# Performance work log

Hardware: AMD Instinct MI355X
Metric: run time of the kernel (lower is better)

The kernel has to match this reference:

```python
import jax, jax.numpy as jnp
import numpy as np

DIM = 512

def setup_inputs() -> dict:
    key = jax.random.key(0)
    k1, k2, k3 = jax.random.split(key, 3)
    context = jax.random.normal(k1, (64, 1024, DIM), dtype=jnp.float32)
    query = jax.random.normal(k2, (64, 128, DIM), dtype=jnp.float32)
    # nn.Linear(3*dim, 1, bias=False) weight, flattened to a (3*dim,) vector
    w0 = jax.random.normal(k3, (3 * DIM,), dtype=jnp.float32) * (1.0 / np.sqrt(3 * DIM))
    return {"context": context, "query": query, "w0": w0}

def reference(context, query, w0):
    # Trilinear similarity: sim[b,i,j] = w_c.c_i + w_q.q_j + w_m.(c_i*q_j)
    # (equivalent to Linear(concat([c, q, c*q])) without materializing the concat)
    d = context.shape[-1]
    wc, wq, wm = w0[:d], w0[d:2 * d], w0[2 * d:]
    sim = (context @ wc)[:, :, None] \
        + (query @ wq)[:, None, :] \
        + jnp.einsum('bid,bjd->bij', context * wm, query)  # (B, ctx, q)
    # Original: softmax over trailing dim of size 1 -> all ones (faithful to the bug)
    S = jnp.ones_like(sim)                 # (B, ctx, q)
    SS = jax.nn.softmax(sim, axis=1)       # softmax over context dim
    A = S @ query                          # (B, ctx, d)
    B = S @ jnp.swapaxes(SS, 1, 2) @ context  # (B, ctx, d)
    return (A, B)
```

## Files before the change

### kernel.cpp

```cpp
#include <hip/hip_runtime.h>
#include <hip/hip_bf16.h>

#define NB   64
#define NC   1024
#define NQ   128
#define DIMD 512
#define BK   64
#define NKC  (DIMD / BK)
#define LDK  (BK + 8)
#define TM   128
#define NTILE (NC / TM)

using short8  = __attribute__((ext_vector_type(8))) short;
using short4v = __attribute__((ext_vector_type(4))) short;
using f32x4   = __attribute__((ext_vector_type(4))) float;
typedef __fp16 half2v __attribute__((ext_vector_type(2)));

__device__ inline float dot4(float4 a, float4 b) {
    return a.x * b.x + a.y * b.y + a.z * b.z + a.w * b.w;
}

__global__ __launch_bounds__(256) void gemm_stats(
    const float* __restrict__ ctx, const float* __restrict__ qry,
    const float* __restrict__ w0, float* __restrict__ stats,
    unsigned short* __restrict__ simh)
{
    __shared__ __attribute__((aligned(16))) short As[TM][LDK];
    __shared__ __attribute__((aligned(16))) short Bs[NQ][LDK];
    __shared__ __attribute__((aligned(16))) float w0L[3 * DIMD];
    __shared__ float cwL[TM], qwL[NQ];
    __shared__ float sL[2][NQ];

    const int tid  = threadIdx.x;
    const int b    = blockIdx.x;
    const int bt   = blockIdx.y;
    const int i0   = bt * TM;
    const int w    = tid >> 6;
    const int lane = tid & 63;
    const int wr   = w >> 1, wcg = w & 1;
    const int RB   = wr * 64, CB = wcg * 64;
    const int n16  = lane & 15, qd = lane >> 4;

    for (int idx = tid; idx < 3 * DIMD; idx += 256) w0L[idx] = w0[idx];

    f32x4 acc[4][4];
#pragma unroll
    for (int ri = 0; ri < 4; ri++)
#pragma unroll
        for (int ci = 0; ci < 4; ci++)
#pragma unroll
            for (int e = 0; e < 4; e++) acc[ri][ci][e] = 0.f;

    const int col4  = n16 * 4;
    const int srow0 = w * 32 + qd;
    const float* cBase = ctx + ((size_t)(b * NC + i0 + srow0)) * DIMD + col4;
    const float* qBase = qry + ((size_t)(b * NQ + srow0)) * DIMD + col4;
    float cwp[8], qwp[8];
#pragma unroll
    for (int u = 0; u < 8; u++) { cwp[u] = 0.f; qwp[u] = 0.f; }

    for (int kc = 0; kc < NKC; kc++) {
        const int k0 = kc * BK;
        __syncthreads();
        float4 wcv = *(const float4*)&w0L[k0 + col4];
        float4 wqv = *(const float4*)&w0L[DIMD + k0 + col4];
        float4 wmv = *(const float4*)&w0L[2 * DIMD + k0 + col4];
#pragma unroll
        for (int u = 0; u < 8; u++) {
            const int row = w * 32 + u * 4 + qd;
            float4 v = *(const float4*)(cBase + k0 + (size_t)u * 4 * DIMD);
            cwp[u] += dot4(v, wcv);
            union { __hip_bfloat162 h[2]; short4v s; } pc;
            pc.h[0] = __float22bfloat162_rn(make_float2(v.x * wmv.x, v.y * wmv.y));
            pc.h[1] = __float22bfloat162_rn(make_float2(v.z * wmv.z, v.w * wmv.w));
            *(short4v*)&As[row][col4] = pc.s;

            float4 q = *(const float4*)(qBase + k0 + (size_t)u * 4 * DIMD);
            qwp[u] += dot4(q, wqv);
            union { __hip_bfloat162 h[2]; short4v s; } pq;
            pq.h[0] = __float22bfloat162_rn(make_float2(q.x, q.y));
            pq.h[1] = __float22bfloat162_rn(make_float2(q.z, q.w));
            *(short4v*)&Bs[row][col4] = pq.s;
        }
        __syncthreads();
#pragma unroll
        for (int ks = 0; ks < BK / 32; ks++) {
            const int kb = ks * 32 + qd * 8;
            short8 af[4], bfr[4];
#pragma unroll
            for (int ri = 0; ri < 4; ri++) af[ri] = *(const short8*)&As[RB + ri * 16 + n16][kb];
#pragma unroll
            for (int ci = 0; ci < 4; ci++) bfr[ci] = *(const short8*)&Bs[CB + ci * 16 + n16][kb];
#pragma unroll
            for (int ri = 0; ri < 4; ri++)
#pragma unroll
                for (int ci = 0; ci < 4; ci++)
                    acc[ri][ci] = __builtin_amdgcn_mfma_f32_16x16x32_bf16(
                        af[ri], bfr[ci], acc[ri][ci], 0, 0, 0);
        }
    }

#pragma unroll
    for (int u = 0; u < 8; u++) {
        float c = cwp[u], q = qwp[u];
#pragma unroll
        for (int off = 1; off < 16; off <<= 1) {
            c += __shfl_xor(c, off);
            q += __shfl_xor(q, off);
        }
        if (n16 == 0) {
            const int row = w * 32 + u * 4 + qd;
            cwL[row] = c; qwL[row] = q;
        }
    }
    __syncthreads();

#pragma unroll
    for (int ci = 0; ci < 4; ci++) {
        const int col = CB + ci * 16 + n16;
        const float qwv = qwL[col];
        unsigned short* simCol = simh + ((size_t)(b * NTILE + bt) * NQ + col) * TM;
        float s = 0.f;
#pragma unroll
        for (int ri = 0; ri < 4; ri++) {
            const int rbase = RB + ri * 16 + qd * 4;
            float v0 = acc[ri][ci][0] + cwL[rbase + 0] + qwv;
            float v1 = acc[ri][ci][1] + cwL[rbase + 1] + qwv;
            float v2 = acc[ri][ci][2] + cwL[rbase + 2] + qwv;
            float v3 = acc[ri][ci][3] + cwL[rbase + 3] + qwv;
            s += __expf(v0) + __expf(v1) + __expf(v2) + __expf(v3);
            half2v h01 = __builtin_amdgcn_cvt_pkrtz(v0, v1);
            half2v h23 = __builtin_amdgcn_cvt_pkrtz(v2, v3);
            uint2 pk;
            pk.x = __builtin_bit_cast(unsigned, h01);
            pk.y = __builtin_bit_cast(unsigned, h23);
            *(uint2*)&simCol[rbase] = pk;
        }
        s += __shfl_xor(s, 16);
        s += __shfl_xor(s, 32);
        if (qd == 0) sL[wr][col] = s;
    }
    __syncthreads();
    if (tid < NQ)
        stats[(size_t)(b * NTILE + bt) * NQ + tid] = sL[0][tid] + sL[1][tid];
}

__global__ void combine_stats(const float* __restrict__ stats, float* __restrict__ colstats)
{
    const int b = blockIdx.x, j = threadIdx.x;
    float s = 0.f;
    for (int t = 0; t < NTILE; t++)
        s += stats[(size_t)(b * NTILE + t) * NQ + j];
    colstats[(size_t)b * NQ + j] = 1.0f / s;
}

__global__ void arow_kernel(const float* __restrict__ qry, float* __restrict__ arow)
{
    const int b = blockIdx.x, h = blockIdx.y;
    const int d = h * 256 + threadIdx.x;
    float a = 0.f;
    const float* base = qry + (size_t)b * NQ * DIMD + d;
    for (int j = 0; j < NQ; j++) a += base[(size_t)j * DIMD];
    arow[(size_t)b * DIMD + d] = a;
}

__global__ __launch_bounds__(256) void rb_kernel(
    const float* __restrict__ ctx, const unsigned short* __restrict__ simh,
    const float* __restrict__ colstats, float* __restrict__ bpart)
{
    __shared__ __attribute__((aligned(16))) unsigned short simL[NQ * TM];
    __shared__ float izL[NQ];
    __shared__ float rpart[2][TM];
    __shared__ float rfin[TM];

    const int tid = threadIdx.x;
    const int b = blockIdx.x, bt = blockIdx.y;
    const int i0 = bt * TM;

    if (tid < NQ) izL[tid] = colstats[(size_t)b * NQ + tid];
    const unsigned short* tileSrc = simh + (size_t)(b * NTILE + bt) * NQ * TM;
#pragma unroll
    for (int it = 0; it < 8; it++) {
        const int idx = (tid + it * 256) * 8;
        *(uint4*)&simL[idx] = *(const uint4*)&tileSrc[idx];
    }
    __syncthreads();

    const int i = tid & 127, jh = tid >> 7;
    float r = 0.f;
    for (int j2 = 0; j2 < 64; j2++) {
        const int j = jh * 64 + j2;
        __fp16 hv = __builtin_bit_cast(__fp16, simL[j * TM + i]);
        r += __expf((float)hv) * izL[j];
    }
    rpart[jh][i] = r;
    __syncthreads();
    if (tid < TM) rfin[tid] = rpart[0][tid] + rpart[1][tid];
    __syncthreads();

    const int d0 = tid * 2;
    float bx = 0.f, by = 0.f;
    const float* cb2 = ctx + ((size_t)b * NC + i0) * DIMD + d0;
    for (int ii = 0; ii < TM; ii++) {
        float  rv = rfin[ii];
        float2 cv = *(const float2*)(cb2 + (size_t)ii * DIMD);
        bx += rv * cv.x; by += rv * cv.y;
    }
    float* bp = bpart + (size_t)(b * NTILE + bt) * DIMD + d0;
    bp[0] = bx; bp[1] = by;
}

__global__ void broadcast_out(const float* __restrict__ arow, const float* __restrict__ bpart,
                              float* __restrict__ out)
{
    const int b = blockIdx.x, ic = blockIdx.y;
    const int t = threadIdx.x;
    const int half = t >> 7;
    const int l = t & 127;
    const int d0 = l * 4;
    float4 val;
    if (half == 0) {
        val = *(const float4*)&arow[(size_t)b * DIMD + d0];
    } else {
        val.x = val.y = val.z = val.w = 0.f;
        for (int t8 = 0; t8 < NTILE; t8++) {
            float4 v = *(const float4*)&bpart[(size_t)(b * NTILE + t8) * DIMD + d0];
            val.x += v.x; val.y += v.y; val.z += v.z; val.w += v.w;
        }
    }
    size_t base = (size_t)half * ((size_t)NB * NC * DIMD)
                + ((size_t)b * NC + (size_t)ic * 32) * DIMD + d0;
    for (int i = 0; i < 32; i++)
        *(float4*)&out[base + (size_t)i * DIMD] = val;
}

extern "C" void kernel_launch(void* const* d_in, const int* in_sizes, int n_in,
                              void* d_out, int out_size, void* d_ws, size_t ws_size,
                              hipStream_t stream)
{
    const float* ctx = (const float*)d_in[0];
    const float* qry = (const float*)d_in[1];
    const float* w0  = (const float*)d_in[2];
    float* out = (float*)d_out;
    float* ws  = (float*)d_ws;

    float* stats    = ws;
    float* colstats = ws + 65536;
    float* arow     = ws + 73728;
    float* bpart    = ws + 106496;
    unsigned short* simh = (unsigned short*)(ws + 524288);

    arow_kernel<<<dim3(NB, 2), 256, 0, stream>>>(qry, arow);
    gemm_stats<<<dim3(NB, NTILE), 256, 0, stream>>>(ctx, qry, w0, stats, simh);
    combine_stats<<<NB, NQ, 0, stream>>>(stats, colstats);
    rb_kernel<<<dim3(NB, NTILE), 256, 0, stream>>>(ctx, simh, colstats, bpart);
    broadcast_out<<<dim3(NB, 32), 256, 0, stream>>>(arow, bpart, out);
}
```

Baseline: 430.4 us.

## Store exp values in fp16, fuse stats combine and query row-sum into rb kernel

After: 416.1 us. 1.03x faster.

```diff
diff --git a/kernel.cpp b/kernel.cpp
--- a/kernel.cpp
+++ b/kernel.cpp
@@ -23,7 +23,7 @@
 __global__ __launch_bounds__(256) void gemm_stats(
     const float* __restrict__ ctx, const float* __restrict__ qry,
     const float* __restrict__ w0, float* __restrict__ stats,
-    unsigned short* __restrict__ simh)
+    unsigned short* __restrict__ eh)
 {
     __shared__ __attribute__((aligned(16))) short As[TM][LDK];
     __shared__ __attribute__((aligned(16))) short Bs[NQ][LDK];
@@ -119,22 +119,22 @@
     for (int ci = 0; ci < 4; ci++) {
         const int col = CB + ci * 16 + n16;
         const float qwv = qwL[col];
-        unsigned short* simCol = simh + ((size_t)(b * NTILE + bt) * NQ + col) * TM;
+        unsigned short* eCol = eh + ((size_t)(b * NTILE + bt) * NQ + col) * TM;
         float s = 0.f;
 #pragma unroll
         for (int ri = 0; ri < 4; ri++) {
             const int rbase = RB + ri * 16 + qd * 4;
-            float v0 = acc[ri][ci][0] + cwL[rbase + 0] + qwv;
-            float v1 = acc[ri][ci][1] + cwL[rbase + 1] + qwv;
-            float v2 = acc[ri][ci][2] + cwL[rbase + 2] + qwv;
-            float v3 = acc[ri][ci][3] + cwL[rbase + 3] + qwv;
-            s += __expf(v0) + __expf(v1) + __expf(v2) + __expf(v3);
-            half2v h01 = __builtin_amdgcn_cvt_pkrtz(v0, v1);
-            half2v h23 = __builtin_amdgcn_cvt_pkrtz(v2, v3);
+            float e0 = __expf(acc[ri][ci][0] + cwL[rbase + 0] + qwv);
+            float e1 = __expf(acc[ri][ci][1] + cwL[rbase + 1] + qwv);
+            float e2 = __expf(acc[ri][ci][2] + cwL[rbase + 2] + qwv);
+            float e3 = __expf(acc[ri][ci][3] + cwL[rbase + 3] + qwv);
+            half2v h01 = __builtin_amdgcn_cvt_pkrtz(e0, e1);
+            half2v h23 = __builtin_amdgcn_cvt_pkrtz(e2, e3);
+            s += (float)h01[0] + (float)h01[1] + (float)h23[0] + (float)h23[1];
             uint2 pk;
             pk.x = __builtin_bit_cast(unsigned, h01);
             pk.y = __builtin_bit_cast(unsigned, h23);
-            *(uint2*)&simCol[rbase] = pk;
+            *(uint2*)&eCol[rbase] = pk;
         }
         s += __shfl_xor(s, 16);
         s += __shfl_xor(s, 32);
@@ -145,44 +145,33 @@
         stats[(size_t)(b * NTILE + bt) * NQ + tid] = sL[0][tid] + sL[1][tid];
 }
 
-__global__ void combine_stats(const float* __restrict__ stats, float* __restrict__ colstats)
-{
-    const int b = blockIdx.x, j = threadIdx.x;
-    float s = 0.f;
-    for (int t = 0; t < NTILE; t++)
-        s += stats[(size_t)(b * NTILE + t) * NQ + j];
-    colstats[(size_t)b * NQ + j] = 1.0f / s;
-}
-
-__global__ void arow_kernel(const float* __restrict__ qry, float* __restrict__ arow)
-{
-    const int b = blockIdx.x, h = blockIdx.y;
-    const int d = h * 256 + threadIdx.x;
-    float a = 0.f;
-    const float* base = qry + (size_t)b * NQ * DIMD + d;
-    for (int j = 0; j < NQ; j++) a += base[(size_t)j * DIMD];
-    arow[(size_t)b * DIMD + d] = a;
-}
-
-__global__ __launch_bounds__(256) void rb_kernel(
-    const float* __restrict__ ctx, const unsigned short* __restrict__ simh,
-    const float* __restrict__ colstats, float* __restrict__ bpart)
-{
-    __shared__ __attribute__((aligned(16))) unsigned short simL[NQ * TM];
+__global__ __launch_bounds__(256) void rb2(
+    const float* __restrict__ ctx, const float* __restrict__ qry,
+    const unsigned short* __restrict__ eh, const float* __restrict__ stats,
+    float* __restrict__ bpart, float* __restrict__ arow)
+{
+    __shared__ __attribute__((aligned(16))) unsigned short eL[NQ * TM];
     __shared__ float izL[NQ];
     __shared__ float rpart[2][TM];
     __shared__ float rfin[TM];
+    __shared__ float qL[4][64];
 
     const int tid = threadIdx.x;
     const int b = blockIdx.x, bt = blockIdx.y;
     const int i0 = bt * TM;
 
-    if (tid < NQ) izL[tid] = colstats[(size_t)b * NQ + tid];
-    const unsigned short* tileSrc = simh + (size_t)(b * NTILE + bt) * NQ * TM;
+    if (tid < NQ) {
+        float ssum = 0.f;
+#pragma unroll
+        for (int t8 = 0; t8 < NTILE; t8++)
+            ssum += stats[(size_t)(b * NTILE + t8) * NQ + tid];
+        izL[tid] = 1.0f / ssum;
+    }
+    const unsigned short* tileSrc = eh + (size_t)(b * NTILE + bt) * NQ * TM;
 #pragma unroll
     for (int it = 0; it < 8; it++) {
         const int idx = (tid + it * 256) * 8;
-        *(uint4*)&simL[idx] = *(const uint4*)&tileSrc[idx];
+        *(uint4*)&eL[idx] = *(const uint4*)&tileSrc[idx];
     }
     __syncthreads();
 
@@ -190,8 +179,8 @@
     float r = 0.f;
     for (int j2 = 0; j2 < 64; j2++) {
         const int j = jh * 64 + j2;
-        __fp16 hv = __builtin_bit_cast(__fp16, simL[j * TM + i]);
-        r += __expf((float)hv) * izL[j];
+        __fp16 hv = __builtin_bit_cast(__fp16, eL[j * TM + i]);
+        r += (float)hv * izL[j];
     }
     rpart[jh][i] = r;
     __syncthreads();
@@ -208,6 +197,17 @@
     }
     float* bp = bpart + (size_t)(b * NTILE + bt) * DIMD + d0;
     bp[0] = bx; bp[1] = by;
+
+    const int dcol = tid & 63, rgrp = tid >> 6;
+    float qs = 0.f;
+    const float* qb = qry + (size_t)b * NQ * DIMD + bt * 64 + dcol;
+    for (int t = 0; t < 32; t++)
+        qs += qb[(size_t)(t * 4 + rgrp) * DIMD];
+    qL[rgrp][dcol] = qs;
+    __syncthreads();
+    if (tid < 64)
+        arow[(size_t)b * DIMD + bt * 64 + tid] =
+            qL[0][tid] + qL[1][tid] + qL[2][tid] + qL[3][tid];
 }
 
 __global__ void broadcast_out(const float* __restrict__ arow, const float* __restrict__ bpart,
@@ -218,20 +218,20 @@
     const int half = t >> 7;
     const int l = t & 127;
     const int d0 = l * 4;
-    float4 val;
+    f32x4 val;
     if (half == 0) {
-        val = *(const float4*)&arow[(size_t)b * DIMD + d0];
+        val = *(const f32x4*)&arow[(size_t)b * DIMD + d0];
     } else {
-        val.x = val.y = val.z = val.w = 0.f;
+        val[0] = val[1] = val[2] = val[3] = 0.f;
         for (int t8 = 0; t8 < NTILE; t8++) {
-            float4 v = *(const float4*)&bpart[(size_t)(b * NTILE + t8) * DIMD + d0];
-            val.x += v.x; val.y += v.y; val.z += v.z; val.w += v.w;
+            f32x4 v = *(const f32x4*)&bpart[(size_t)(b * NTILE + t8) * DIMD + d0];
+            val[0] += v[0]; val[1] += v[1]; val[2] += v[2]; val[3] += v[3];
         }
     }
     size_t base = (size_t)half * ((size_t)NB * NC * DIMD)
                 + ((size_t)b * NC + (size_t)ic * 32) * DIMD + d0;
     for (int i = 0; i < 32; i++)
-        *(float4*)&out[base + (size_t)i * DIMD] = val;
+        __builtin_nontemporal_store(val, (f32x4*)&out[base + (size_t)i * DIMD]);
 }
 
 extern "C" void kernel_launch(void* const* d_in, const int* in_sizes, int n_in,
@@ -244,15 +244,12 @@
     float* out = (float*)d_out;
     float* ws  = (float*)d_ws;
 
-    float* stats    = ws;
-    float* colstats = ws + 65536;
-    float* arow     = ws + 73728;
-    float* bpart    = ws + 106496;
-    unsigned short* simh = (unsigned short*)(ws + 524288);
-
-    arow_kernel<<<dim3(NB, 2), 256, 0, stream>>>(qry, arow);
-    gemm_stats<<<dim3(NB, NTILE), 256, 0, stream>>>(ctx, qry, w0, stats, simh);
-    combine_stats<<<NB, NQ, 0, stream>>>(stats, colstats);
-    rb_kernel<<<dim3(NB, NTILE), 256, 0, stream>>>(ctx, simh, colstats, bpart);
+    float* stats = ws;
+    float* arow  = ws + 65536;
+    float* bpart = ws + 98304;
+    unsigned short* eh = (unsigned short*)(ws + 360448);
+
+    gemm_stats<<<dim3(NB, NTILE), 256, 0, stream>>>(ctx, qry, w0, stats, eh);
+    rb2<<<dim3(NB, NTILE), 256, 0, stream>>>(ctx, qry, eh, stats, bpart, arow);
     broadcast_out<<<dim3(NB, 32), 256, 0, stream>>>(arow, bpart, out);
 }
```
